# Performance work log

Measured on AMD Instinct MI355X. Metric: run time of the kernel, lower is better.

The kernel has to match this reference:

```python
import jax, jax.numpy as jnp
import numpy as np

B, T, H, NH, K = 8, 1024, 1024, 16, 3
HD = H // NH
EPS = 1e-5


def _ln(x, g, b):
    m = jnp.mean(x, axis=-1, keepdims=True)
    v = jnp.mean((x - m) ** 2, axis=-1, keepdims=True)
    return (x - m) * jax.lax.rsqrt(v + EPS) * g + b


def _ffn(x, g, b, w1, b1, w2, b2):
    h = jax.nn.gelu(_ln(x, g, b) @ w1 + b1, approximate=False)
    return h @ w2 + b2


def setup_inputs() -> dict:
    key = jax.random.key(0)
    ks = jax.random.split(key, 10)
    s = 0.02
    d = {}
    d['x'] = jax.random.normal(ks[0], (B, T, H), jnp.float32)
    d['ln1_g'] = jnp.ones((H,), jnp.float32); d['ln1_b'] = jnp.zeros((H,), jnp.float32)
    d['ffn1_w1'] = jax.random.normal(ks[1], (H, 2 * H), jnp.float32) * s
    d['ffn1_b1'] = jnp.zeros((2 * H,), jnp.float32)
    d['ffn1_w2'] = jax.random.normal(ks[2], (2 * H, H), jnp.float32) * s
    d['ffn1_b2'] = jnp.zeros((H,), jnp.float32)
    d['an_g'] = jnp.ones((H,), jnp.float32); d['an_b'] = jnp.zeros((H,), jnp.float32)
    d['qkv_w'] = jax.random.normal(ks[3], (H, 3 * H), jnp.float32) * s
    d['qkv_b'] = jnp.zeros((3 * H,), jnp.float32)
    d['out_w'] = jax.random.normal(ks[4], (H, H), jnp.float32) * s
    d['out_b'] = jnp.zeros((H,), jnp.float32)
    d['cn_g'] = jnp.ones((H,), jnp.float32); d['cn_b'] = jnp.zeros((H,), jnp.float32)
    d['dw_k'] = jax.random.normal(ks[5], (H, 1, K), jnp.float32) * s  # depthwise [O,I/g,K]
    d['dw_b'] = jnp.zeros((H,), jnp.float32)
    d['pw_w'] = jax.random.normal(ks[6], (H, H), jnp.float32) * s  # pointwise [out,in]
    d['pw_b'] = jnp.zeros((H,), jnp.float32)
    d['ln2_g'] = jnp.ones((H,), jnp.float32); d['ln2_b'] = jnp.zeros((H,), jnp.float32)
    d['ffn2_w1'] = jax.random.normal(ks[7], (H, 2 * H), jnp.float32) * s
    d['ffn2_b1'] = jnp.zeros((2 * H,), jnp.float32)
    d['ffn2_w2'] = jax.random.normal(ks[8], (2 * H, H), jnp.float32) * s
    d['ffn2_b2'] = jnp.zeros((H,), jnp.float32)
    return d


def reference(x, ln1_g, ln1_b, ffn1_w1, ffn1_b1, ffn1_w2, ffn1_b2,
              an_g, an_b, qkv_w, qkv_b, out_w, out_b,
              cn_g, cn_b, dw_k, dw_b, pw_w, pw_b,
              ln2_g, ln2_b, ffn2_w1, ffn2_b1, ffn2_w2, ffn2_b2):
    # macaron FFN 1
    x = x + 0.5 * _ffn(x, ln1_g, ln1_b, ffn1_w1, ffn1_b1, ffn1_w2, ffn1_b2)

    # causal self-attention (pre-norm)
    h = _ln(x, an_g, an_b)
    qkv = (h @ qkv_w + qkv_b).reshape(B, T, 3, NH, HD)
    q, k, v = qkv[:, :, 0], qkv[:, :, 1], qkv[:, :, 2]  # [B,T,NH,HD]
    scale = 1.0 / np.sqrt(HD).astype(np.float32)
    scores = jnp.einsum('bqhd,bkhd->bhqk', q, k) * scale  # [B,NH,T,T]
    causal = jnp.tril(jnp.ones((T, T), dtype=bool))
    scores = jnp.where(causal[None, None], scores, -jnp.inf)
    attn = jax.nn.softmax(scores, axis=-1)
    o = jnp.einsum('bhqk,bkhd->bqhd', attn, v).reshape(B, T, H)
    x = x + (o @ out_w + out_b)

    # conv module: LN -> causal depthwise conv(k=3) -> GELU -> pointwise conv
    c = _ln(x, cn_g, cn_b).transpose(0, 2, 1)  # [B,H,T]
    c = jnp.pad(c, ((0, 0), (0, 0), (K - 1, 0)))  # causal left pad
    c = jax.lax.conv_general_dilated(
        c, dw_k, window_strides=(1,), padding='VALID',
        dimension_numbers=('NCH', 'OIH', 'NCH'), feature_group_count=H)
    c = c + dw_b[None, :, None]
    c = jax.nn.gelu(c, approximate=False)
    c = jnp.einsum('oc,bct->bot', pw_w, c) + pw_b[None, :, None]  # 1x1 conv
    x = x + c.transpose(0, 2, 1)

    # macaron FFN 2
    x = x + 0.5 * _ffn(x, ln2_g, ln2_b, ffn2_w1, ffn2_b1, ffn2_w2, ffn2_b2)
    return x
```

## Files before the change

### kernel.cpp

```cpp
#include <hip/hip_runtime.h>
#include <hip/hip_bf16.h>
#include <math.h>

typedef __bf16 bf16;
typedef __bf16 bf16x8 __attribute__((ext_vector_type(8)));
typedef float  f32x4  __attribute__((ext_vector_type(4)));

#define B_   8
#define T_   1024
#define H_   1024
#define MTOK (B_ * T_)

static __device__ __forceinline__ float gelu_f(float x) {
    return 0.5f * x * (1.0f + erff(x * 0.70710678118654752f));
}

__global__ __launch_bounds__(256)
void transpose_cast_k(const float* __restrict__ in, bf16* __restrict__ out,
                      int Kd, int Nd)
{
    __shared__ float tile[32][33];
    int n0 = blockIdx.x * 32;
    int k0 = blockIdx.y * 32;
    int tx = threadIdx.x & 31, ty = threadIdx.x >> 5;
#pragma unroll
    for (int i = 0; i < 32; i += 8)
        tile[ty + i][tx] = in[(size_t)(k0 + ty + i) * Nd + n0 + tx];
    __syncthreads();
#pragma unroll
    for (int i = 0; i < 32; i += 8)
        out[(size_t)(n0 + ty + i) * Kd + k0 + tx] = (bf16)tile[tx][ty + i];
}

__global__ __launch_bounds__(256)
void cast_k(const float* __restrict__ in, bf16* __restrict__ out)
{
    int i = blockIdx.x * 256 + threadIdx.x;
    float4 v = ((const float4*)in)[i];
    bf16* o = out + (size_t)i * 4;
    o[0] = (bf16)v.x; o[1] = (bf16)v.y; o[2] = (bf16)v.z; o[3] = (bf16)v.w;
}

__global__ __launch_bounds__(256)
void ln_k(const float* __restrict__ x, const float* __restrict__ g,
          const float* __restrict__ b, bf16* __restrict__ out)
{
    int row = blockIdx.x;
    float4 v = ((const float4*)(x + (size_t)row * H_))[threadIdx.x];
    float s  = v.x + v.y + v.z + v.w;
    float s2 = v.x * v.x + v.y * v.y + v.z * v.z + v.w * v.w;
#pragma unroll
    for (int off = 32; off > 0; off >>= 1) {
        s  += __shfl_down(s, off);
        s2 += __shfl_down(s2, off);
    }
    __shared__ float red[8];
    int wave = threadIdx.x >> 6, lane = threadIdx.x & 63;
    if (lane == 0) { red[wave] = s; red[wave + 4] = s2; }
    __syncthreads();
    s  = red[0] + red[1] + red[2] + red[3];
    s2 = red[4] + red[5] + red[6] + red[7];
    float mean = s * (1.0f / H_);
    float var  = s2 * (1.0f / H_) - mean * mean;
    float rstd = rsqrtf(var + 1e-5f);
    int c = threadIdx.x * 4;
    float4 gv = *(const float4*)(g + c);
    float4 bv = *(const float4*)(b + c);
    bf16* o = out + (size_t)row * H_ + c;
    o[0] = (bf16)((v.x - mean) * rstd * gv.x + bv.x);
    o[1] = (bf16)((v.y - mean) * rstd * gv.y + bv.y);
    o[2] = (bf16)((v.z - mean) * rstd * gv.z + bv.z);
    o[3] = (bf16)((v.w - mean) * rstd * gv.w + bv.w);
}

__global__ __launch_bounds__(256)
void dwconv_k(const bf16* __restrict__ cl, const float* __restrict__ kw,
              const float* __restrict__ kb, bf16* __restrict__ out)
{
    size_t idx = (size_t)blockIdx.x * 256 + threadIdx.x;
    int ch = (int)(idx & (H_ - 1));
    int t  = (int)((idx >> 10) & (T_ - 1));
    float acc = kb[ch];
    float w0 = kw[ch * 3 + 0], w1 = kw[ch * 3 + 1], w2 = kw[ch * 3 + 2];
    acc += (float)cl[idx] * w2;
    if (t >= 1) acc += (float)cl[idx - H_] * w1;
    if (t >= 2) acc += (float)cl[idx - 2 * H_] * w0;
    out[idx] = (bf16)gelu_f(acc);
}

#define BM 128
#define BN 128
#define BK 32
#define LDK 40

template<int EPI>
__global__ __launch_bounds__(256)
void gemm_k(const bf16* __restrict__ A, const bf16* __restrict__ WT,
            const float* __restrict__ bias, const float* __restrict__ res,
            float* __restrict__ outF, bf16* __restrict__ outB,
            int N, int K)
{
    __shared__ bf16 As[BM * LDK];
    __shared__ bf16 Bs[BN * LDK];
    const int tid  = threadIdx.x;
    const int wave = tid >> 6;
    const int lane = tid & 63;
    const int quad = lane >> 4;
    const int lr   = lane & 15;
    const int bm = blockIdx.x * BM;
    const int bn = blockIdx.y * BN;
    const int wm = (wave & 1) * 64;
    const int wn = (wave >> 1) * 64;

    f32x4 acc[4][4];
#pragma unroll
    for (int mi = 0; mi < 4; mi++)
#pragma unroll
        for (int ni = 0; ni < 4; ni++)
#pragma unroll
            for (int r = 0; r < 4; r++) acc[mi][ni][r] = 0.f;

    for (int k0 = 0; k0 < K; k0 += BK) {
#pragma unroll
        for (int i = 0; i < 2; i++) {
            int c = tid + i * 256;
            int row = c >> 2;
            int col = (c & 3) << 3;
            *(bf16x8*)(&As[row * LDK + col]) =
                *(const bf16x8*)(&A[(size_t)(bm + row) * K + k0 + col]);
            *(bf16x8*)(&Bs[row * LDK + col]) =
                *(const bf16x8*)(&WT[(size_t)(bn + row) * K + k0 + col]);
        }
        __syncthreads();
        bf16x8 af[4], bfr[4];
#pragma unroll
        for (int mi = 0; mi < 4; mi++)
            af[mi] = *(const bf16x8*)(&As[(wm + mi * 16 + lr) * LDK + quad * 8]);
#pragma unroll
        for (int ni = 0; ni < 4; ni++)
            bfr[ni] = *(const bf16x8*)(&Bs[(wn + ni * 16 + lr) * LDK + quad * 8]);
#pragma unroll
        for (int mi = 0; mi < 4; mi++)
#pragma unroll
            for (int ni = 0; ni < 4; ni++)
                acc[mi][ni] = __builtin_amdgcn_mfma_f32_16x16x32_bf16(
                    af[mi], bfr[ni], acc[mi][ni], 0, 0, 0);
        __syncthreads();
    }

#pragma unroll
    for (int mi = 0; mi < 4; mi++) {
#pragma unroll
        for (int ni = 0; ni < 4; ni++) {
            int col = bn + wn + ni * 16 + lr;
            float bv = bias[col];
#pragma unroll
            for (int r = 0; r < 4; r++) {
                int row = bm + wm + mi * 16 + quad * 4 + r;
                size_t idx = (size_t)row * N + col;
                float v = acc[mi][ni][r] + bv;
                if (EPI == 0)      outB[idx] = (bf16)gelu_f(v);
                else if (EPI == 1) outB[idx] = (bf16)v;
                else if (EPI == 2) outF[idx] = v + res[idx];
                else               outF[idx] = res[idx] + 0.5f * v;
            }
        }
    }
}

#define ASTR 72

__global__ __launch_bounds__(256)
void attn_k(const bf16* __restrict__ qkv, bf16* __restrict__ o)
{
    const int qt = blockIdx.x;
    const int bh = blockIdx.y;
    const int b = bh >> 4, h = bh & 15;
    const int tid  = threadIdx.x;
    const int wave = tid >> 6, lane = tid & 63;
    const int quad = lane >> 4, lr = lane & 15;
    const int wq = wave * 16;

    __shared__ bf16 Qs[64 * ASTR];
    __shared__ bf16 Ks[64 * ASTR];
    __shared__ bf16 Vt[64 * ASTR];
    __shared__ bf16 Ps[4][16 * ASTR];

    const size_t base = (size_t)b * T_ * 3072;

#pragma unroll
    for (int i = 0; i < 2; i++) {
        int c = tid + i * 256;
        int row = c >> 3, ch = (c & 7) << 3;
        *(bf16x8*)(&Qs[row * ASTR + ch]) =
            *(const bf16x8*)(&qkv[base + (size_t)(qt * 64 + row) * 3072 + h * 64 + ch]);
    }
    __syncthreads();
    bf16x8 qf[2];
    qf[0] = *(const bf16x8*)(&Qs[(wq + lr) * ASTR + quad * 8]);
    qf[1] = *(const bf16x8*)(&Qs[(wq + lr) * ASTR + 32 + quad * 8]);

    f32x4 oacc[4];
    float m_run[4], l_run[4];
#pragma unroll
    for (int ni = 0; ni < 4; ni++)
#pragma unroll
        for (int r = 0; r < 4; r++) oacc[ni][r] = 0.f;
#pragma unroll
    for (int r = 0; r < 4; r++) { m_run[r] = -INFINITY; l_run[r] = 0.f; }

    for (int kt = 0; kt <= qt; kt++) {
        __syncthreads();
#pragma unroll
        for (int i = 0; i < 2; i++) {
            int c = tid + i * 256;
            int row = c >> 3, ch = (c & 7) << 3;
            *(bf16x8*)(&Ks[row * ASTR + ch]) =
                *(const bf16x8*)(&qkv[base + (size_t)(kt * 64 + row) * 3072 + 1024 + h * 64 + ch]);
            bf16x8 vv =
                *(const bf16x8*)(&qkv[base + (size_t)(kt * 64 + row) * 3072 + 2048 + h * 64 + ch]);
#pragma unroll
            for (int j = 0; j < 8; j++)
                Vt[(ch + j) * ASTR + row] = vv[j];
        }
        __syncthreads();

        f32x4 sv[4];
#pragma unroll
        for (int ni = 0; ni < 4; ni++) {
            bf16x8 kf0 = *(const bf16x8*)(&Ks[(ni * 16 + lr) * ASTR + quad * 8]);
            bf16x8 kf1 = *(const bf16x8*)(&Ks[(ni * 16 + lr) * ASTR + 32 + quad * 8]);
            f32x4 t;
#pragma unroll
            for (int r = 0; r < 4; r++) t[r] = 0.f;
            t = __builtin_amdgcn_mfma_f32_16x16x32_bf16(qf[0], kf0, t, 0, 0, 0);
            t = __builtin_amdgcn_mfma_f32_16x16x32_bf16(qf[1], kf1, t, 0, 0, 0);
            sv[ni] = t;
        }

        const int gq_base = qt * 64 + wq + quad * 4;
        const int gs_base = kt * 64 + lr;
        float rmax[4];
#pragma unroll
        for (int r = 0; r < 4; r++) rmax[r] = -INFINITY;
#pragma unroll
        for (int ni = 0; ni < 4; ni++)
#pragma unroll
            for (int r = 0; r < 4; r++) {
                float xv = sv[ni][r] * 0.125f;
                if (gs_base + ni * 16 > gq_base + r) xv = -INFINITY;
                sv[ni][r] = xv;
                rmax[r] = fmaxf(rmax[r], xv);
            }
#pragma unroll
        for (int off = 1; off < 16; off <<= 1)
#pragma unroll
            for (int r = 0; r < 4; r++)
                rmax[r] = fmaxf(rmax[r], __shfl_xor(rmax[r], off));

        float alpha[4], rsum[4];
#pragma unroll
        for (int r = 0; r < 4; r++) {
            float mn = fmaxf(m_run[r], rmax[r]);
            alpha[r] = __expf(m_run[r] - mn);
            m_run[r] = mn;
            rsum[r] = 0.f;
        }
#pragma unroll
        for (int ni = 0; ni < 4; ni++)
#pragma unroll
            for (int r = 0; r < 4; r++) {
                float p = __expf(sv[ni][r] - m_run[r]);
                rsum[r] += p;
                Ps[wave][(quad * 4 + r) * ASTR + ni * 16 + lr] = (bf16)p;
            }
#pragma unroll
        for (int off = 1; off < 16; off <<= 1)
#pragma unroll
            for (int r = 0; r < 4; r++)
                rsum[r] += __shfl_xor(rsum[r], off);
#pragma unroll
        for (int r = 0; r < 4; r++)
            l_run[r] = l_run[r] * alpha[r] + rsum[r];
#pragma unroll
        for (int ni = 0; ni < 4; ni++)
#pragma unroll
            for (int r = 0; r < 4; r++)
                oacc[ni][r] *= alpha[r];

        bf16x8 pf0 = *(const bf16x8*)(&Ps[wave][lr * ASTR + quad * 8]);
        bf16x8 pf1 = *(const bf16x8*)(&Ps[wave][lr * ASTR + 32 + quad * 8]);
#pragma unroll
        for (int ni = 0; ni < 4; ni++) {
            bf16x8 vf0 = *(const bf16x8*)(&Vt[(ni * 16 + lr) * ASTR + quad * 8]);
            bf16x8 vf1 = *(const bf16x8*)(&Vt[(ni * 16 + lr) * ASTR + 32 + quad * 8]);
            oacc[ni] = __builtin_amdgcn_mfma_f32_16x16x32_bf16(pf0, vf0, oacc[ni], 0, 0, 0);
            oacc[ni] = __builtin_amdgcn_mfma_f32_16x16x32_bf16(pf1, vf1, oacc[ni], 0, 0, 0);
        }
    }

#pragma unroll
    for (int r = 0; r < 4; r++) {
        float inv = 1.0f / l_run[r];
        int gq = qt * 64 + wq + quad * 4 + r;
#pragma unroll
        for (int ni = 0; ni < 4; ni++)
            o[((size_t)(b * T_ + gq)) * H_ + h * 64 + ni * 16 + lr] =
                (bf16)(oacc[ni][r] * inv);
    }
}

extern "C" void kernel_launch(void* const* d_in, const int* in_sizes, int n_in,
                              void* d_out, int out_size, void* d_ws, size_t ws_size,
                              hipStream_t stream)
{
    const float* x_in  = (const float*)d_in[0];
    const float* ln1_g = (const float*)d_in[1];
    const float* ln1_b = (const float*)d_in[2];
    const float* f1w1  = (const float*)d_in[3];
    const float* f1b1  = (const float*)d_in[4];
    const float* f1w2  = (const float*)d_in[5];
    const float* f1b2  = (const float*)d_in[6];
    const float* an_g  = (const float*)d_in[7];
    const float* an_b  = (const float*)d_in[8];
    const float* qkv_w = (const float*)d_in[9];
    const float* qkv_b = (const float*)d_in[10];
    const float* out_w = (const float*)d_in[11];
    const float* out_b = (const float*)d_in[12];
    const float* cn_g  = (const float*)d_in[13];
    const float* cn_b  = (const float*)d_in[14];
    const float* dw_k  = (const float*)d_in[15];
    const float* dw_b  = (const float*)d_in[16];
    const float* pw_w  = (const float*)d_in[17];
    const float* pw_b  = (const float*)d_in[18];
    const float* ln2_g = (const float*)d_in[19];
    const float* ln2_b = (const float*)d_in[20];
    const float* f2w1  = (const float*)d_in[21];
    const float* f2b1  = (const float*)d_in[22];
    const float* f2w2  = (const float*)d_in[23];
    const float* f2b2  = (const float*)d_in[24];
    float* outp = (float*)d_out;

    char* ws = (char*)d_ws;
    size_t off = 0;
    auto alloc = [&](size_t bytes) {
        char* p = ws + off;
        off += (bytes + 255) & ~(size_t)255;
        return p;
    };
    bf16* w1T_1 = (bf16*)alloc(2048ULL * 1024 * 2);
    bf16* w2T_1 = (bf16*)alloc(1024ULL * 2048 * 2);
    bf16* qkvT  = (bf16*)alloc(3072ULL * 1024 * 2);
    bf16* outT  = (bf16*)alloc(1024ULL * 1024 * 2);
    bf16* pwB   = (bf16*)alloc(1024ULL * 1024 * 2);
    bf16* w1T_2 = (bf16*)alloc(2048ULL * 1024 * 2);
    bf16* w2T_2 = (bf16*)alloc(1024ULL * 2048 * 2);
    bf16* bufa  = (bf16*)alloc((size_t)MTOK * 1024 * 2);
    bf16* gbuf  = (bf16*)alloc((size_t)MTOK * 1024 * 2);
    bf16* hid   = (bf16*)alloc((size_t)MTOK * 3072 * 2);
    float* xw   = (float*)alloc((size_t)MTOK * 1024 * 4);

    transpose_cast_k<<<dim3(64, 32), 256, 0, stream>>>(f1w1, w1T_1, 1024, 2048);
    transpose_cast_k<<<dim3(32, 64), 256, 0, stream>>>(f1w2, w2T_1, 2048, 1024);
    transpose_cast_k<<<dim3(96, 32), 256, 0, stream>>>(qkv_w, qkvT, 1024, 3072);
    transpose_cast_k<<<dim3(32, 32), 256, 0, stream>>>(out_w, outT, 1024, 1024);
    transpose_cast_k<<<dim3(64, 32), 256, 0, stream>>>(f2w1, w1T_2, 1024, 2048);
    transpose_cast_k<<<dim3(32, 64), 256, 0, stream>>>(f2w2, w2T_2, 2048, 1024);
    cast_k<<<1024, 256, 0, stream>>>(pw_w, pwB);

    ln_k<<<MTOK, 256, 0, stream>>>(x_in, ln1_g, ln1_b, bufa);
    gemm_k<0><<<dim3(64, 16), 256, 0, stream>>>(bufa, w1T_1, f1b1, nullptr, nullptr, hid, 2048, 1024);
    gemm_k<3><<<dim3(64, 8), 256, 0, stream>>>(hid, w2T_1, f1b2, x_in, xw, nullptr, 1024, 2048);

    ln_k<<<MTOK, 256, 0, stream>>>(xw, an_g, an_b, bufa);
    gemm_k<1><<<dim3(64, 24), 256, 0, stream>>>(bufa, qkvT, qkv_b, nullptr, nullptr, hid, 3072, 1024);
    attn_k<<<dim3(16, 128), 256, 0, stream>>>(hid, bufa);
    gemm_k<2><<<dim3(64, 8), 256, 0, stream>>>(bufa, outT, out_b, xw, xw, nullptr, 1024, 1024);

    ln_k<<<MTOK, 256, 0, stream>>>(xw, cn_g, cn_b, bufa);
    dwconv_k<<<MTOK * 1024 / 256, 256, 0, stream>>>(bufa, dw_k, dw_b, gbuf);
    gemm_k<2><<<dim3(64, 8), 256, 0, stream>>>(gbuf, pwB, pw_b, xw, xw, nullptr, 1024, 1024);

    ln_k<<<MTOK, 256, 0, stream>>>(xw, ln2_g, ln2_b, bufa);
    gemm_k<0><<<dim3(64, 16), 256, 0, stream>>>(bufa, w1T_2, f2b1, nullptr, nullptr, hid, 2048, 1024);
    gemm_k<3><<<dim3(64, 8), 256, 0, stream>>>(hid, w2T_2, f2b2, xw, outp, nullptr, 1024, 2048);
}
```

Baseline: 789.7 us.

## Use direct global-to-LDS loads in GEMM and pre-transpose V for attention

The GEMM tile loads now use global_load_lds (16-byte direct-to-LDS async copies) instead of register round-trips, and the LDS padding is dropped so tiles are contiguous. Attention no longer transposes V element-by-element into shared memory inside every key-tile iteration. A separate kernel writes V transposed into a scratch buffer once, and attention loads it with vector copies. The costs are an extra kernel launch, extra global traffic for the V copy, and possible LDS bank conflicts now that the GEMM tiles are unpadded.

```diff
diff --git a/kernel.cpp b/kernel.cpp
--- a/kernel.cpp
+++ b/kernel.cpp
@@ -15,6 +15,12 @@
     return 0.5f * x * (1.0f + erff(x * 0.70710678118654752f));
 }
 
+static __device__ __forceinline__ void async16(const bf16* g, bf16* l) {
+    __builtin_amdgcn_global_load_lds(
+        (const __attribute__((address_space(1))) void*)g,
+        (__attribute__((address_space(3))) void*)l, 16, 0, 0);
+}
+
 __global__ __launch_bounds__(256)
 void transpose_cast_k(const float* __restrict__ in, bf16* __restrict__ out,
                       int Kd, int Nd)
@@ -39,6 +45,33 @@
     float4 v = ((const float4*)in)[i];
     bf16* o = out + (size_t)i * 4;
     o[0] = (bf16)v.x; o[1] = (bf16)v.y; o[2] = (bf16)v.z; o[3] = (bf16)v.w;
+}
+
+__global__ __launch_bounds__(256)
+void transpose_v_k(const bf16* __restrict__ qkv, bf16* __restrict__ vt)
+{
+    __shared__ bf16 tile[64][72];
+    const int t0 = blockIdx.x * 64;
+    const int bh = blockIdx.y;
+    const int b = bh >> 4, h = bh & 15;
+    const int tid = threadIdx.x;
+#pragma unroll
+    for (int i = 0; i < 2; i++) {
+        int c = tid + i * 256;
+        int row = c >> 3, ch = (c & 7) << 3;
+        *(bf16x8*)(&tile[row][ch]) =
+            *(const bf16x8*)(&qkv[(size_t)(b * T_ + t0 + row) * 3072 + 2048 + h * 64 + ch]);
+    }
+    __syncthreads();
+#pragma unroll
+    for (int i = 0; i < 2; i++) {
+        int c = tid + i * 256;
+        int hd = c >> 3, tc = (c & 7) << 3;
+        bf16x8 v;
+#pragma unroll
+        for (int j = 0; j < 8; j++) v[j] = tile[tc + j][hd];
+        *(bf16x8*)(&vt[((size_t)bh * 64 + hd) * T_ + t0 + tc]) = v;
+    }
 }
 
 __global__ __launch_bounds__(256)
@@ -91,7 +124,6 @@
 #define BM 128
 #define BN 128
 #define BK 32
-#define LDK 40
 
 template<int EPI>
 __global__ __launch_bounds__(256)
@@ -100,8 +132,8 @@
             float* __restrict__ outF, bf16* __restrict__ outB,
             int N, int K)
 {
-    __shared__ bf16 As[BM * LDK];
-    __shared__ bf16 Bs[BN * LDK];
+    __shared__ bf16 As[BM * BK];
+    __shared__ bf16 Bs[BN * BK];
     const int tid  = threadIdx.x;
     const int wave = tid >> 6;
     const int lane = tid & 63;
@@ -112,6 +144,9 @@
     const int wm = (wave & 1) * 64;
     const int wn = (wave >> 1) * 64;
 
+    const int crow = lane >> 2;
+    const int ccol = (lane & 3) << 3;
+
     f32x4 acc[4][4];
 #pragma unroll
     for (int mi = 0; mi < 4; mi++)
@@ -122,23 +157,19 @@
 
     for (int k0 = 0; k0 < K; k0 += BK) {
 #pragma unroll
-        for (int i = 0; i < 2; i++) {
-            int c = tid + i * 256;
-            int row = c >> 2;
-            int col = (c & 3) << 3;
-            *(bf16x8*)(&As[row * LDK + col]) =
-                *(const bf16x8*)(&A[(size_t)(bm + row) * K + k0 + col]);
-            *(bf16x8*)(&Bs[row * LDK + col]) =
-                *(const bf16x8*)(&WT[(size_t)(bn + row) * K + k0 + col]);
+        for (int t = 0; t < 2; t++) {
+            const int c = wave * 2 + t;
+            async16(&A[(size_t)(bm + c * 16 + crow) * K + k0 + ccol], &As[c * 512]);
+            async16(&WT[(size_t)(bn + c * 16 + crow) * K + k0 + ccol], &Bs[c * 512]);
         }
         __syncthreads();
         bf16x8 af[4], bfr[4];
 #pragma unroll
         for (int mi = 0; mi < 4; mi++)
-            af[mi] = *(const bf16x8*)(&As[(wm + mi * 16 + lr) * LDK + quad * 8]);
-#pragma unroll
-        for (int ni = 0; ni < 4; ni++)
-            bfr[ni] = *(const bf16x8*)(&Bs[(wn + ni * 16 + lr) * LDK + quad * 8]);
+            af[mi] = *(const bf16x8*)(&As[(wm + mi * 16 + lr) * BK + quad * 8]);
+#pragma unroll
+        for (int ni = 0; ni < 4; ni++)
+            bfr[ni] = *(const bf16x8*)(&Bs[(wn + ni * 16 + lr) * BK + quad * 8]);
 #pragma unroll
         for (int mi = 0; mi < 4; mi++)
 #pragma unroll
@@ -171,7 +202,8 @@
 #define ASTR 72
 
 __global__ __launch_bounds__(256)
-void attn_k(const bf16* __restrict__ qkv, bf16* __restrict__ o)
+void attn_k(const bf16* __restrict__ qkv, const bf16* __restrict__ vt,
+            bf16* __restrict__ o)
 {
     const int qt = blockIdx.x;
     const int bh = blockIdx.y;
@@ -183,10 +215,11 @@
 
     __shared__ bf16 Qs[64 * ASTR];
     __shared__ bf16 Ks[64 * ASTR];
-    __shared__ bf16 Vt[64 * ASTR];
+    __shared__ bf16 Vts[64 * ASTR];
     __shared__ bf16 Ps[4][16 * ASTR];
 
     const size_t base = (size_t)b * T_ * 3072;
+    const size_t vtbase = (size_t)bh * 64 * T_;
 
 #pragma unroll
     for (int i = 0; i < 2; i++) {
@@ -217,11 +250,8 @@
             int row = c >> 3, ch = (c & 7) << 3;
             *(bf16x8*)(&Ks[row * ASTR + ch]) =
                 *(const bf16x8*)(&qkv[base + (size_t)(kt * 64 + row) * 3072 + 1024 + h * 64 + ch]);
-            bf16x8 vv =
-                *(const bf16x8*)(&qkv[base + (size_t)(kt * 64 + row) * 3072 + 2048 + h * 64 + ch]);
-#pragma unroll
-            for (int j = 0; j < 8; j++)
-                Vt[(ch + j) * ASTR + row] = vv[j];
+            *(bf16x8*)(&Vts[row * ASTR + ch]) =
+                *(const bf16x8*)(&vt[vtbase + (size_t)row * T_ + kt * 64 + ch]);
         }
         __syncthreads();
 
@@ -292,8 +322,8 @@
         bf16x8 pf1 = *(const bf16x8*)(&Ps[wave][lr * ASTR + 32 + quad * 8]);
 #pragma unroll
         for (int ni = 0; ni < 4; ni++) {
-            bf16x8 vf0 = *(const bf16x8*)(&Vt[(ni * 16 + lr) * ASTR + quad * 8]);
-            bf16x8 vf1 = *(const bf16x8*)(&Vt[(ni * 16 + lr) * ASTR + 32 + quad * 8]);
+            bf16x8 vf0 = *(const bf16x8*)(&Vts[(ni * 16 + lr) * ASTR + quad * 8]);
+            bf16x8 vf1 = *(const bf16x8*)(&Vts[(ni * 16 + lr) * ASTR + 32 + quad * 8]);
             oacc[ni] = __builtin_amdgcn_mfma_f32_16x16x32_bf16(pf0, vf0, oacc[ni], 0, 0, 0);
             oacc[ni] = __builtin_amdgcn_mfma_f32_16x16x32_bf16(pf1, vf1, oacc[ni], 0, 0, 0);
         }
@@ -359,6 +389,7 @@
     bf16* gbuf  = (bf16*)alloc((size_t)MTOK * 1024 * 2);
     bf16* hid   = (bf16*)alloc((size_t)MTOK * 3072 * 2);
     float* xw   = (float*)alloc((size_t)MTOK * 1024 * 4);
+    bf16* vt    = gbuf;
 
     transpose_cast_k<<<dim3(64, 32), 256, 0, stream>>>(f1w1, w1T_1, 1024, 2048);
     transpose_cast_k<<<dim3(32, 64), 256, 0, stream>>>(f1w2, w2T_1, 2048, 1024);
@@ -374,7 +405,8 @@
 
     ln_k<<<MTOK, 256, 0, stream>>>(xw, an_g, an_b, bufa);
     gemm_k<1><<<dim3(64, 24), 256, 0, stream>>>(bufa, qkvT, qkv_b, nullptr, nullptr, hid, 3072, 1024);
-    attn_k<<<dim3(16, 128), 256, 0, stream>>>(hid, bufa);
+    transpose_v_k<<<dim3(16, 128), 256, 0, stream>>>(hid, vt);
+    attn_k<<<dim3(16, 128), 256, 0, stream>>>(hid, vt, bufa);
     gemm_k<2><<<dim3(64, 8), 256, 0, stream>>>(bufa, outT, out_b, xw, xw, nullptr, 1024, 1024);
 
     ln_k<<<MTOK, 256, 0, stream>>>(xw, cn_g, cn_b, bufa);
```

After: 743.7 us. 5.8% less time.
